# Kernel tuning notes

Measured on AMD Instinct MI355X. Metric: run time of the kernel, lower is better.

## Reference

```python
import jax, jax.numpy as jnp
import numpy as np


def setup_inputs() -> dict:
    key = jax.random.key(0)
    k1, k2 = jax.random.split(key)
    x = jax.random.normal(k1, (16, 64, 224, 224), dtype=jnp.float32)
    # conv weight [out=1, in=2, kh=7, kw=7]; init roughly mimics small-normal init
    conv_w = jax.random.normal(k2, (1, 2, 7, 7), dtype=jnp.float32) * 0.01
    conv_b = jnp.zeros((1,), dtype=jnp.float32)
    return {"x": x, "conv_w": conv_w, "conv_b": conv_b}


def reference(x, conv_w, conv_b):
    # channel-wise mean and max -> [B, 2, H, W]
    avg_out = jnp.mean(x, axis=1, keepdims=True)
    max_out = jnp.max(x, axis=1, keepdims=True)
    feat = jnp.concatenate([avg_out, max_out], axis=1)
    # 2->1 channel 7x7 conv, padding 3 (same)
    y = jax.lax.conv_general_dilated(
        feat, conv_w,
        window_strides=(1, 1),
        padding=((3, 3), (3, 3)),
        dimension_numbers=("NCHW", "OIHW", "NCHW"),
    ) + conv_b[None, :, None, None]
    # sigmoid gate broadcast-multiplied back onto x
    return jax.nn.sigmoid(y) * x
```

## Files before the change

kernel.cpp:

```cpp
#include <hip/hip_runtime.h>
#include <math.h>

#define BB 16
#define CC 64
#define HH 224
#define WW 224
#define HWSZ (HH * WW)
#define HW4 (HWSZ / 4)
#define W4 (WW / 4)

#define PROWS (HH + 6)
#define PW4 60
#define PPLANE (PROWS * PW4)
#define NPADC 1256
#define NPADT (BB * NPADC)

typedef float f32x4 __attribute__((ext_vector_type(4)));

#define TA 256
#define NPIX (BB * HW4)
#define NBLKA (NPIX / TA)

__global__ __launch_bounds__(TA) void reduce_kernel(const float* __restrict__ x,
                                                    float* __restrict__ feat) {
    const int idx = blockIdx.x * TA + threadIdx.x;
    const int b   = idx / HW4;
    const int p   = idx - b * HW4;
    const f32x4* xp = reinterpret_cast<const f32x4*>(x) + (size_t)b * (CC * HW4) + p;

    f32x4 s = {0.f, 0.f, 0.f, 0.f};
    f32x4 m = {-INFINITY, -INFINITY, -INFINITY, -INFINITY};
#pragma unroll 16
    for (int c = 0; c < CC; ++c) {
        f32x4 u = xp[(size_t)c * HW4];
        s += u;
        m[0] = fmaxf(m[0], u[0]); m[1] = fmaxf(m[1], u[1]);
        m[2] = fmaxf(m[2], u[2]); m[3] = fmaxf(m[3], u[3]);
    }

    f32x4* fa4 = reinterpret_cast<f32x4*>(feat);
    f32x4* fm4 = fa4 + (size_t)BB * PPLANE;

    const int h  = p / W4;
    const int w4 = p - h * W4;
    const size_t o = (size_t)(b * PROWS + (h + 3)) * PW4 + (w4 + 2);
    fa4[o] = s * (1.0f / 64.0f);
    fm4[o] = m;

    if (idx < NPADT) {
        const int pb = idx / NPADC;
        int r = idx - pb * NPADC;
        int prow, c4;
        if (r < 360) {
            int rr = r / 60;
            c4 = r - rr * 60;
            prow = (rr < 3) ? rr : 224 + rr;
        } else {
            int r2 = r - 360;
            int rw = r2 >> 2;
            int k  = r2 & 3;
            prow = rw + 3;
            c4 = (k < 2) ? k : 56 + k;
        }
        const size_t oz = (size_t)(pb * PROWS + prow) * PW4 + c4;
        f32x4 z = {0.f, 0.f, 0.f, 0.f};
        fa4[oz] = z;
        fm4[oz] = z;
    }
}

#define TCN 256
#define SEGS (WW / 8)
#define NTHC (BB * HH * SEGS)
#define NBLKC (NTHC / TCN)

__global__ __launch_bounds__(TCN) void conv_kernel(const float* __restrict__ feat,
                                                   const float* __restrict__ cw,
                                                   const float* __restrict__ cb,
                                                   float* __restrict__ gate) {
    const int tid = blockIdx.x * TCN + threadIdx.x;
    const int b   = tid / (HH * SEGS);
    const int r   = tid - b * (HH * SEGS);
    const int row = r / SEGS;
    const int seg = r - row * SEGS;
    const int w0  = seg * 8;

    float wa[49], wb[49];
#pragma unroll
    for (int i = 0; i < 49; ++i) { wa[i] = cw[i]; wb[i] = cw[49 + i]; }
    const float bias = cb[0];

    const f32x4* fab = reinterpret_cast<const f32x4*>(feat) + (size_t)b * PPLANE;
    const f32x4* fmb = fab + (size_t)BB * PPLANE;

    float acc[8];
#pragma unroll
    for (int j = 0; j < 8; ++j) acc[j] = bias;

#pragma unroll
    for (int kh = 0; kh < 7; ++kh) {
        const int bi = (row + kh) * PW4 + seg * 2 + 1;
        float fA[16], fM[16];
#pragma unroll
        for (int q = 0; q < 4; ++q) {
            f32x4 a = fab[bi + q];
            f32x4 mm = fmb[bi + q];
#pragma unroll
            for (int e = 0; e < 4; ++e) { fA[q * 4 + e] = a[e]; fM[q * 4 + e] = mm[e]; }
        }
#pragma unroll
        for (int kw = 0; kw < 7; ++kw) {
            const float w1 = wa[kh * 7 + kw];
            const float w2 = wb[kh * 7 + kw];
#pragma unroll
            for (int j = 0; j < 8; ++j) {
                acc[j] = fmaf(fA[1 + kw + j], w1, acc[j]);
                acc[j] = fmaf(fM[1 + kw + j], w2, acc[j]);
            }
        }
    }

    f32x4 g0, g1;
#pragma unroll
    for (int j = 0; j < 4; ++j) g0[j] = 1.0f / (1.0f + expf(-acc[j]));
#pragma unroll
    for (int j = 0; j < 4; ++j) g1[j] = 1.0f / (1.0f + expf(-acc[4 + j]));

    f32x4* gb = reinterpret_cast<f32x4*>(gate) + ((size_t)b * HWSZ + (size_t)row * WW + w0) / 4;
    gb[0] = g0;
    gb[1] = g1;
}

#define TM 256
#define CSPL 4
#define CPG (CC / CSPL)
#define CHUNKS (HW4 / TM)
#define NBLKM (BB * CSPL * CHUNKS)

__global__ __launch_bounds__(TM) void mul_kernel(const float* __restrict__ x,
                                                 const float* __restrict__ gate,
                                                 float* __restrict__ out) {
    const int blk   = blockIdx.x;
    const int chunk = blk % CHUNKS;
    const int cg    = (blk / CHUNKS) % CSPL;
    const int b     = blk / (CHUNKS * CSPL);
    const int p     = chunk * TM + threadIdx.x;

    const f32x4 g = reinterpret_cast<const f32x4*>(gate)[(size_t)b * HW4 + p];

    const size_t base = ((size_t)b * CC + cg * CPG) * HW4 + p;
    const f32x4* xp = reinterpret_cast<const f32x4*>(x) + base;
    f32x4*       op = reinterpret_cast<f32x4*>(out) + base;
#pragma unroll
    for (int c = 0; c < CPG; ++c) {
        f32x4 v = xp[(size_t)c * HW4];
        v *= g;
        op[(size_t)c * HW4] = v;
    }
}

extern "C" void kernel_launch(void* const* d_in, const int* in_sizes, int n_in,
                              void* d_out, int out_size, void* d_ws, size_t ws_size,
                              hipStream_t stream) {
    const float* x  = (const float*)d_in[0];
    const float* cw = (const float*)d_in[1];
    const float* cb = (const float*)d_in[2];
    float* out  = (float*)d_out;
    float* feat = (float*)d_ws;
    float* gate = feat + (size_t)2 * BB * PPLANE * 4;

    reduce_kernel<<<NBLKA, TA, 0, stream>>>(x, feat);
    conv_kernel<<<NBLKC, TCN, 0, stream>>>(feat, cw, cb, gate);
    mul_kernel<<<NBLKM, TM, 0, stream>>>(x, gate, out);
}
```

Baseline: 392.4 us.

## Fuse conv and gating multiply, split channel reduction across warps

The 7x7 conv and the sigmoid-gate multiply now run in one kernel. Each block computes the gate for its pixels and applies it to half of the channels, so the gate buffer write and re-read and one launch go away. The conv work is done twice, once per channel half. The reduce kernel now splits the 64 channels across four wave groups per 64-pixel block, combines them through shared memory, and moves the border zero-padding into separate blocks. This raises memory-level parallelism in the reduction, at the cost of a barrier and a serial shared-memory combine step.

```diff
diff --git a/kernel.cpp b/kernel.cpp
--- a/kernel.cpp
+++ b/kernel.cpp
@@ -19,90 +19,123 @@
 
 #define TA 256
 #define NPIX (BB * HW4)
-#define NBLKA (NPIX / TA)
+#define PIXBLK 64
+#define NBLKA_MAIN (NPIX / PIXBLK)
+#define NBLKA_PAD ((NPADT + TA - 1) / TA)
+#define NBLKA (NBLKA_MAIN + NBLKA_PAD)
 
 __global__ __launch_bounds__(TA) void reduce_kernel(const float* __restrict__ x,
                                                     float* __restrict__ feat) {
-    const int idx = blockIdx.x * TA + threadIdx.x;
-    const int b   = idx / HW4;
-    const int p   = idx - b * HW4;
-    const f32x4* xp = reinterpret_cast<const f32x4*>(x) + (size_t)b * (CC * HW4) + p;
+    __shared__ f32x4 sS[4][PIXBLK];
+    __shared__ f32x4 sM[4][PIXBLK];
 
-    f32x4 s = {0.f, 0.f, 0.f, 0.f};
-    f32x4 m = {-INFINITY, -INFINITY, -INFINITY, -INFINITY};
-#pragma unroll 16
-    for (int c = 0; c < CC; ++c) {
-        f32x4 u = xp[(size_t)c * HW4];
-        s += u;
-        m[0] = fmaxf(m[0], u[0]); m[1] = fmaxf(m[1], u[1]);
-        m[2] = fmaxf(m[2], u[2]); m[3] = fmaxf(m[3], u[3]);
-    }
-
+    const int blk = blockIdx.x;
+    const int t   = threadIdx.x;
     f32x4* fa4 = reinterpret_cast<f32x4*>(feat);
     f32x4* fm4 = fa4 + (size_t)BB * PPLANE;
 
-    const int h  = p / W4;
-    const int w4 = p - h * W4;
-    const size_t o = (size_t)(b * PROWS + (h + 3)) * PW4 + (w4 + 2);
-    fa4[o] = s * (1.0f / 64.0f);
-    fm4[o] = m;
+    if (blk < NBLKA_MAIN) {
+        const int P0    = blk * PIXBLK;
+        const int bimg  = P0 / HW4;
+        const int pbase = P0 - bimg * HW4;
+        const int lane  = t & 63;
+        const int cg    = t >> 6;
+        const int p     = pbase + lane;
 
-    if (idx < NPADT) {
-        const int pb = idx / NPADC;
-        int r = idx - pb * NPADC;
-        int prow, c4;
-        if (r < 360) {
-            int rr = r / 60;
-            c4 = r - rr * 60;
-            prow = (rr < 3) ? rr : 224 + rr;
-        } else {
-            int r2 = r - 360;
-            int rw = r2 >> 2;
-            int k  = r2 & 3;
-            prow = rw + 3;
-            c4 = (k < 2) ? k : 56 + k;
+        const f32x4* xp = reinterpret_cast<const f32x4*>(x)
+                        + ((size_t)(bimg * CC + cg * 16)) * HW4 + p;
+        f32x4 s = {0.f, 0.f, 0.f, 0.f};
+        f32x4 m = {-INFINITY, -INFINITY, -INFINITY, -INFINITY};
+#pragma unroll 8
+        for (int c = 0; c < 16; ++c) {
+            f32x4 u = xp[(size_t)c * HW4];
+            s += u;
+            m[0] = fmaxf(m[0], u[0]); m[1] = fmaxf(m[1], u[1]);
+            m[2] = fmaxf(m[2], u[2]); m[3] = fmaxf(m[3], u[3]);
         }
-        const size_t oz = (size_t)(pb * PROWS + prow) * PW4 + c4;
-        f32x4 z = {0.f, 0.f, 0.f, 0.f};
-        fa4[oz] = z;
-        fm4[oz] = z;
+        sS[cg][lane] = s;
+        sM[cg][lane] = m;
+        __syncthreads();
+
+        if (t < PIXBLK) {
+            f32x4 r = sS[0][t] + sS[1][t] + sS[2][t] + sS[3][t];
+            const int pp = pbase + t;
+            const int h  = pp / W4;
+            const int w4 = pp - h * W4;
+            fa4[(size_t)(bimg * PROWS + h + 3) * PW4 + (w4 + 2)] = r * (1.0f / 64.0f);
+        } else if (t < 2 * PIXBLK) {
+            const int l = t - PIXBLK;
+            f32x4 a = sM[0][l], b2 = sM[1][l], c2 = sM[2][l], d = sM[3][l];
+            f32x4 r;
+#pragma unroll
+            for (int e = 0; e < 4; ++e)
+                r[e] = fmaxf(fmaxf(a[e], b2[e]), fmaxf(c2[e], d[e]));
+            const int pp = pbase + l;
+            const int h  = pp / W4;
+            const int w4 = pp - h * W4;
+            fm4[(size_t)(bimg * PROWS + h + 3) * PW4 + (w4 + 2)] = r;
+        }
+    } else {
+        const int idx = (blk - NBLKA_MAIN) * TA + t;
+        if (idx < NPADT) {
+            const int pb = idx / NPADC;
+            int r = idx - pb * NPADC;
+            int prow, c4;
+            if (r < 360) {
+                int rr = r / 60;
+                c4 = r - rr * 60;
+                prow = (rr < 3) ? rr : 224 + rr;
+            } else {
+                int r2 = r - 360;
+                int rw = r2 >> 2;
+                int k  = r2 & 3;
+                prow = rw + 3;
+                c4 = (k < 2) ? k : 56 + k;
+            }
+            const size_t oz = (size_t)(pb * PROWS + prow) * PW4 + c4;
+            f32x4 z = {0.f, 0.f, 0.f, 0.f};
+            fa4[oz] = z;
+            fm4[oz] = z;
+        }
     }
 }
 
-#define TCN 256
-#define SEGS (WW / 8)
-#define NTHC (BB * HH * SEGS)
-#define NBLKC (NTHC / TCN)
+#define TB 256
+#define BSPL 2
+#define CPG2 (CC / BSPL)
+#define CHB (HW4 / TB)
+#define NBLKB (BB * BSPL * CHB)
 
-__global__ __launch_bounds__(TCN) void conv_kernel(const float* __restrict__ feat,
-                                                   const float* __restrict__ cw,
-                                                   const float* __restrict__ cb,
-                                                   float* __restrict__ gate) {
-    const int tid = blockIdx.x * TCN + threadIdx.x;
-    const int b   = tid / (HH * SEGS);
-    const int r   = tid - b * (HH * SEGS);
-    const int row = r / SEGS;
-    const int seg = r - row * SEGS;
-    const int w0  = seg * 8;
+__global__ __launch_bounds__(TB) void conv_mul_kernel(const float* __restrict__ x,
+                                                      const float* __restrict__ feat,
+                                                      const float* __restrict__ cw,
+                                                      const float* __restrict__ cb,
+                                                      float* __restrict__ out) {
+    __shared__ float ws[98];
 
-    float wa[49], wb[49];
-#pragma unroll
-    for (int i = 0; i < 49; ++i) { wa[i] = cw[i]; wb[i] = cw[49 + i]; }
-    const float bias = cb[0];
+    const int blk = blockIdx.x;
+    const int t   = threadIdx.x;
+    if (t < 98) ws[t] = cw[t];
+
+    const int chunk = blk % CHB;
+    const int half  = (blk / CHB) % BSPL;
+    const int b     = blk / (CHB * BSPL);
+    const int p     = chunk * TB + t;
+    const int row   = p / W4;
+    const int c4    = p - row * W4;
+    __syncthreads();
 
     const f32x4* fab = reinterpret_cast<const f32x4*>(feat) + (size_t)b * PPLANE;
     const f32x4* fmb = fab + (size_t)BB * PPLANE;
+    const float bias = cb[0];
 
-    float acc[8];
+    float acc[4] = {bias, bias, bias, bias};
+#pragma unroll 1
+    for (int kh = 0; kh < 7; ++kh) {
+        const int bi = (row + kh) * PW4 + c4 + 1;
+        float fA[12], fM[12];
 #pragma unroll
-    for (int j = 0; j < 8; ++j) acc[j] = bias;
-
-#pragma unroll
-    for (int kh = 0; kh < 7; ++kh) {
-        const int bi = (row + kh) * PW4 + seg * 2 + 1;
-        float fA[16], fM[16];
-#pragma unroll
-        for (int q = 0; q < 4; ++q) {
+        for (int q = 0; q < 3; ++q) {
             f32x4 a = fab[bi + q];
             f32x4 mm = fmb[bi + q];
 #pragma unroll
@@ -110,49 +143,25 @@
         }
 #pragma unroll
         for (int kw = 0; kw < 7; ++kw) {
-            const float w1 = wa[kh * 7 + kw];
-            const float w2 = wb[kh * 7 + kw];
+            const float w1 = ws[kh * 7 + kw];
+            const float w2 = ws[49 + kh * 7 + kw];
 #pragma unroll
-            for (int j = 0; j < 8; ++j) {
+            for (int j = 0; j < 4; ++j) {
                 acc[j] = fmaf(fA[1 + kw + j], w1, acc[j]);
                 acc[j] = fmaf(fM[1 + kw + j], w2, acc[j]);
             }
         }
     }
 
-    f32x4 g0, g1;
+    f32x4 g;
 #pragma unroll
-    for (int j = 0; j < 4; ++j) g0[j] = 1.0f / (1.0f + expf(-acc[j]));
-#pragma unroll
-    for (int j = 0; j < 4; ++j) g1[j] = 1.0f / (1.0f + expf(-acc[4 + j]));
+    for (int j = 0; j < 4; ++j) g[j] = 1.0f / (1.0f + expf(-acc[j]));
 
-    f32x4* gb = reinterpret_cast<f32x4*>(gate) + ((size_t)b * HWSZ + (size_t)row * WW + w0) / 4;
-    gb[0] = g0;
-    gb[1] = g1;
-}
-
-#define TM 256
-#define CSPL 4
-#define CPG (CC / CSPL)
-#define CHUNKS (HW4 / TM)
-#define NBLKM (BB * CSPL * CHUNKS)
-
-__global__ __launch_bounds__(TM) void mul_kernel(const float* __restrict__ x,
-                                                 const float* __restrict__ gate,
-                                                 float* __restrict__ out) {
-    const int blk   = blockIdx.x;
-    const int chunk = blk % CHUNKS;
-    const int cg    = (blk / CHUNKS) % CSPL;
-    const int b     = blk / (CHUNKS * CSPL);
-    const int p     = chunk * TM + threadIdx.x;
-
-    const f32x4 g = reinterpret_cast<const f32x4*>(gate)[(size_t)b * HW4 + p];
-
-    const size_t base = ((size_t)b * CC + cg * CPG) * HW4 + p;
+    const size_t base = ((size_t)(b * CC + half * CPG2)) * HW4 + p;
     const f32x4* xp = reinterpret_cast<const f32x4*>(x) + base;
     f32x4*       op = reinterpret_cast<f32x4*>(out) + base;
-#pragma unroll
-    for (int c = 0; c < CPG; ++c) {
+#pragma unroll 8
+    for (int c = 0; c < CPG2; ++c) {
         f32x4 v = xp[(size_t)c * HW4];
         v *= g;
         op[(size_t)c * HW4] = v;
@@ -167,9 +176,7 @@
     const float* cb = (const float*)d_in[2];
     float* out  = (float*)d_out;
     float* feat = (float*)d_ws;
-    float* gate = feat + (size_t)2 * BB * PPLANE * 4;
 
     reduce_kernel<<<NBLKA, TA, 0, stream>>>(x, feat);
-    conv_kernel<<<NBLKC, TCN, 0, stream>>>(feat, cw, cb, gate);
-    mul_kernel<<<NBLKM, TM, 0, stream>>>(x, gate, out);
+    conv_mul_kernel<<<NBLKB, TB, 0, stream>>>(x, feat, cw, cb, out);
 }
```

Measured after the change: 392.2 us. Within noise of the previous version (-0.0%).
